# Kernel optimization log

Hardware: AMD Instinct MI355X
Metric: run time of the kernel (lower is better)

## Reference

```python
import jax, jax.numpy as jnp
import numpy as np

N = 10000      # nodes
E = 320000     # edges (avg degree 32)
H = 128        # hidden_channels
G = 50         # num_gaussians
NF = 128       # num_filters
L = 6          # num_interactions
CUTOFF = 10.0


def ssp(x):
    # ShiftedSoftplus: softplus(x) - log(2)
    return jax.nn.softplus(x) - jnp.log(2.0).astype(x.dtype)


def setup_inputs() -> dict:
    key = jax.random.key(0)
    ks = jax.random.split(key, 16)
    s = 0.05
    return {
        "z": jax.random.normal(ks[0], (N, H), jnp.float32),
        "pos": jax.random.normal(ks[1], (N, 3), jnp.float32) * 3.0,
        "edge_index": jax.random.randint(ks[2], (2, E), 0, N, dtype=jnp.int64),
        # per-layer stacked parameters (PyTorch Linear convention: y = x @ W.T + b)
        "mlp1_w": jax.random.normal(ks[3], (L, NF, G), jnp.float32) * s,
        "mlp1_b": jnp.zeros((L, NF), jnp.float32),
        "mlp2_w": jax.random.normal(ks[4], (L, NF, NF), jnp.float32) * s,
        "mlp2_b": jnp.zeros((L, NF), jnp.float32),
        "lin1_w": jax.random.normal(ks[5], (L, NF, H), jnp.float32) * s,   # no bias
        "lin2_w": jax.random.normal(ks[6], (L, H, NF), jnp.float32) * s,
        "lin2_b": jnp.zeros((L, H), jnp.float32),
        "lin_w": jax.random.normal(ks[7], (L, H, H), jnp.float32) * s,
        "lin_b": jnp.zeros((L, H), jnp.float32),
        "coord_w": jax.random.normal(ks[8], (L, 1, G + 2 * H), jnp.float32) * s,
        "coord_b": jnp.zeros((L, 1), jnp.float32),
    }


def reference(z, pos, edge_index, mlp1_w, mlp1_b, mlp2_w, mlp2_b,
              lin1_w, lin2_w, lin2_b, lin_w, lin_b, coord_w, coord_b):
    row, col = edge_index[0], edge_index[1]
    # edge distances from INITIAL positions (computed once, as in torch code)
    edge_weight = jnp.linalg.norm(pos[row] - pos[col], axis=-1)          # [E]
    offset = jnp.linspace(0.0, CUTOFF, G).astype(pos.dtype)              # [G]
    coeff = -0.5 / (offset[1] - offset[0]) ** 2
    edge_attr = jnp.exp(coeff * (edge_weight[:, None] - offset[None, :]) ** 2)  # [E,G]
    C = 0.5 * (jnp.cos(edge_weight * jnp.pi / CUTOFF) + 1.0)             # [E] cosine cutoff
    ones_e = jnp.ones((E,), pos.dtype)
    h = z
    for l in range(L):
        # ---- coordinate update (uses current pos and current h) ----
        feat = jnp.concatenate([edge_attr, h[row], h[col]], axis=-1)     # [E, G+2H]
        cw = feat @ coord_w[l].T + coord_b[l]                            # [E,1]
        aggr = (pos[row] - pos[col]) * cw                                # [E,3]
        sums = jax.ops.segment_sum(aggr, row, num_segments=N)            # [N,3]
        cnt = jax.ops.segment_sum(ones_e, row, num_segments=N)           # [N]
        mean = jnp.where(cnt[:, None] > 0, sums / jnp.maximum(cnt, 1.0)[:, None], 0.0)
        pos = pos + mean
        # ---- CFConv interaction ----
        Wf = ssp(edge_attr @ mlp1_w[l].T + mlp1_b[l]) @ mlp2_w[l].T + mlp2_b[l]  # [E,NF]
        Wf = Wf * C[:, None]
        xf = h @ lin1_w[l].T                                             # [N,NF]
        agg = jax.ops.segment_sum(xf[row] * Wf, col, num_segments=N)     # [N,NF]
        out = agg @ lin2_w[l].T + lin2_b[l]                              # [N,H]
        h = h + (ssp(out) @ lin_w[l].T + lin_b[l])
    return (pos, h)
```

## Files before the change

### kernel.cpp

```cpp
#include <hip/hip_runtime.h>


#define NN 10000
#define EE 320000
#define HH 128
#define GG 50
#define NF 128
#define NL 6
#define TROWS 2048
#define NB 128

typedef unsigned short u16;
typedef unsigned int u32;
typedef short bf16x8 __attribute__((ext_vector_type(8)));
typedef float f32x4  __attribute__((ext_vector_type(4)));

__device__ __forceinline__ float us2f(u16 u){
  union { float f; u32 i; } v; v.i = ((u32)u) << 16; return v.f;
}
__device__ __forceinline__ u16 f2us(float x){
  union { float f; u32 i; } v; v.f = x;
  u32 r = v.i + 0x7fffu + ((v.i >> 16) & 1u);
  return (u16)(r >> 16);
}
__device__ __forceinline__ float ldin(const void* p, int i, int bf){
  return bf ? us2f(((const u16*)p)[i]) : ((const float*)p)[i];
}
__device__ __forceinline__ float sspf(float x){
  return fmaxf(x, 0.f) + __logf(1.f + __expf(-fabsf(x))) - 0.6931472f;
}
__device__ __forceinline__ int detect_bf(const u32* __restrict__ zraw){
  int lane = threadIdx.x & 63;
  int c = 0;
  #pragma unroll
  for(int j=0;j<4;j++){
    u32 w = zraw[lane*4+j];
    u32 hb = (w >> 8) & 0x7F;
    c += (hb >= 0x38 && hb <= 0x41) ? 1 : 0;
  }
  return __popcll(__ballot(c >= 2)) >= 32;
}
__device__ __forceinline__ int detect_i64(const int* __restrict__ ei_raw){
  int lane = threadIdx.x & 63;
  int c = 0;
  #pragma unroll
  for(int j=0;j<4;j++) c += (ei_raw[2*(lane*4+j)+1] == 0) ? 1 : 0;
  return __popcll(__ballot(c >= 3)) >= 32;
}

__global__ void k_prep(const u32* __restrict__ zraw, const void* __restrict__ pos_in,
    const void* __restrict__ mlp1_w, const void* __restrict__ mlp1_b,
    const void* __restrict__ mlp2_w, const void* __restrict__ mlp2_b,
    const void* __restrict__ lin1_w, const void* __restrict__ lin2_w,
    const void* __restrict__ lin2_b, const void* __restrict__ lin_w,
    const void* __restrict__ lin_b,  const void* __restrict__ coord_w,
    const void* __restrict__ coord_b,
    float* __restrict__ h, float* __restrict__ pos, int* __restrict__ wmaxi,
    float* __restrict__ b1f, float* __restrict__ b2v,
    float* __restrict__ w1t, float* __restrict__ w2t,
    float* __restrict__ l1t, u16* __restrict__ l1b, u16* __restrict__ l2b,
    float* __restrict__ l2bf, u16* __restrict__ lwb,
    float* __restrict__ lbf, float* __restrict__ cwf, float* __restrict__ cbf)
{
  int bf = detect_bf(zraw);
  int b = blockIdx.x;
  if(b < NN*HH/256){
    int i = b*256 + threadIdx.x;
    h[i] = ldin(zraw, i, bf);
    if(i < NN*3) pos[i] = ldin(pos_in, i, bf);
    if(i == 0) *wmaxi = 0;
  } else {
    int i = (b - NN*HH/256)*256 + threadIdx.x;
    if(i < NL*NF){
      b1f[i]  = ldin(mlp1_b, i, bf);
      b2v[i]  = ldin(mlp2_b, i, bf);
      l2bf[i] = ldin(lin2_b, i, bf);
      lbf[i]  = ldin(lin_b,  i, bf);
    }
    if(i < NL*GG*NF){
      int l = i/(GG*NF), rem = i%(GG*NF);
      int g = rem/NF, f = rem%NF;
      w1t[i] = ldin(mlp1_w, (l*NF + f)*GG + g, bf);
    }
    if(i < NL*NF*NF){
      int l = i/(NF*NF), rem = i%(NF*NF);
      int k = rem/NF, f = rem%NF;
      w2t[i] = ldin(mlp2_w, l*NF*NF + f*NF + k, bf);
      l1t[i] = ldin(lin1_w, l*NF*HH + f*HH + k, bf);
      l1b[i] = f2us(ldin(lin1_w, i, bf));
      l2b[i] = f2us(ldin(lin2_w, i, bf));
      lwb[i] = f2us(ldin(lin_w,  i, bf));
    }
    if(i < NL*(GG+2*HH)) cwf[i] = ldin(coord_w, i, bf);
    if(i < NL) cbf[i] = ldin(coord_b, i, bf);
  }
}

__global__ void k_count(const int* __restrict__ ei_raw, const float* __restrict__ pos,
                        int* __restrict__ eiN, float* __restrict__ wE,
                        u32* __restrict__ partR32, u32* __restrict__ partC32,
                        int* __restrict__ wmaxi){
  __shared__ u32 hr[NN/2];
  __shared__ u32 hc[NN/2];
  int is64 = detect_i64(ei_raw);
  int b = blockIdx.x, tid = threadIdx.x;
  for(int i=tid; i<NN/2; i+=256){ hr[i]=0; hc[i]=0; }
  __syncthreads();
  int e0 = b*(EE/NB), e1 = e0 + EE/NB;
  float wm = 0.f;
  for(int e = e0 + tid; e < e1; e += 256){
    int r = is64 ? ei_raw[2*e] : ei_raw[e];
    int c = is64 ? ei_raw[2*(EE+e)] : ei_raw[EE+e];
    eiN[e] = r; eiN[EE+e] = c;
    float dx = pos[r*3+0]-pos[c*3+0];
    float dy = pos[r*3+1]-pos[c*3+1];
    float dz = pos[r*3+2]-pos[c*3+2];
    float w = sqrtf(dx*dx + dy*dy + dz*dz);
    wE[e] = w;
    wm = fmaxf(wm, w);
    atomicAdd(&hr[r>>1], (r&1) ? 0x10000u : 1u);
    atomicAdd(&hc[c>>1], (c&1) ? 0x10000u : 1u);
  }
  #pragma unroll
  for(int s=32; s>0; s>>=1) wm = fmaxf(wm, __shfl_down(wm, s, 64));
  if((tid & 63) == 0) atomicMax(wmaxi, __float_as_int(wm));
  __syncthreads();
  for(int i=tid; i<NN/2; i+=256){
    partR32[(size_t)b*(NN/2) + i] = hr[i];
    partC32[(size_t)b*(NN/2) + i] = hc[i];
  }
}

__global__ void k_sumpref(u16* __restrict__ partR16, u16* __restrict__ partC16,
                          int* __restrict__ degR, int* __restrict__ degC){
  int n = blockIdx.x*256 + threadIdx.x;
  if(n >= NN) return;
  u32 rr = 0, rc = 0;
  for(int b=0; b<NB; b++){
    u32 vr = partR16[(size_t)b*NN + n], vc = partC16[(size_t)b*NN + n];
    partR16[(size_t)b*NN + n] = (u16)rr;
    partC16[(size_t)b*NN + n] = (u16)rc;
    rr += vr; rc += vc;
  }
  degR[n] = (int)rr; degC[n] = (int)rc;
}

__global__ void k_scan2(const int* __restrict__ col_deg, const int* __restrict__ deg_row,
                        int* __restrict__ col_start, int* __restrict__ row_start){
  __shared__ int part[1024];
  int tid = threadIdx.x;
  const int CH = (NN + 1023)/1024;
  for(int pass=0; pass<2; pass++){
    const int* deg = pass ? deg_row : col_deg;
    int* start = pass ? row_start : col_start;
    int base = tid*CH;
    int s = 0;
    for(int i=0;i<CH;i++){ int idx=base+i; if(idx<NN) s += deg[idx]; }
    part[tid] = s;
    __syncthreads();
    for(int off=1; off<1024; off<<=1){
      int v = (tid>=off) ? part[tid-off] : 0;
      __syncthreads();
      part[tid] += v;
      __syncthreads();
    }
    int run = (tid==0) ? 0 : part[tid-1];
    for(int i=0;i<CH;i++){
      int idx = base+i;
      if(idx<NN){ start[idx]=run; run += deg[idx]; }
    }
    if(tid==1023) start[NN] = run;
    __syncthreads();
  }
}

__global__ void k_fill(const int* __restrict__ eiN, const float* __restrict__ wE,
                       const int* __restrict__ col_start, const int* __restrict__ row_start,
                       const u16* __restrict__ partR16, const u16* __restrict__ partC16,
                       int* __restrict__ row_s, float* __restrict__ wEs,
                       int* __restrict__ rcol_s, float* __restrict__ rw_s){
  __shared__ u32 hr[NN/2];
  __shared__ u32 hc[NN/2];
  int b = blockIdx.x, t = threadIdx.x;
  for(int i=t; i<NN/2; i+=256){ hr[i]=0; hc[i]=0; }
  __syncthreads();
  int e0 = b*(EE/NB), e1 = e0 + EE/NB;
  for(int e = e0 + t; e < e1; e += 256){
    int r = eiN[e], c = eiN[EE+e];
    float w = wE[e];
    u32 oldc = atomicAdd(&hc[c>>1], (c&1) ? 0x10000u : 1u);
    u32 rkc = (c&1) ? (oldc >> 16) : (oldc & 0xFFFFu);
    int p = col_start[c] + (int)partC16[(size_t)b*NN + c] + (int)rkc;
    row_s[p] = r; wEs[p] = w;
    u32 oldr = atomicAdd(&hr[r>>1], (r&1) ? 0x10000u : 1u);
    u32 rkr = (r&1) ? (oldr >> 16) : (oldr & 0xFFFFu);
    int p2 = row_start[r] + (int)partR16[(size_t)b*NN + r] + (int)rkr;
    rcol_s[p2] = c; rw_s[p2] = w;
  }
}

__global__ void k_tabnode(const float* __restrict__ w1t, const float* __restrict__ b1f,
                          const float* __restrict__ w2t, const float* __restrict__ b2v,
                          const float* __restrict__ cwf, const int* __restrict__ wmaxi,
                          u32* __restrict__ tabGb, float* __restrict__ tabS,
                          const float* __restrict__ h, const float* __restrict__ l1t,
                          u16* __restrict__ xfb0, float* __restrict__ dr0,
                          float* __restrict__ dc0){
  __shared__ float attr[17*64];
  __shared__ float tls[128*19];
  int b = blockIdx.x, t = threadIdx.x;
  if(b < NL*128){
    int l = b >> 7;
    int r0 = (b & 127)*16;
    int f = t & 127, half = t >> 7;
    float delta = __int_as_float(*wmaxi) / (float)(TROWS-1);
    for(int idx=t; idx<17*64; idx+=256){
      int r = idx >> 6, g = idx & 63;
      int row = min(r0 + r, TROWS-1);
      float w = (float)row*delta;
      float d = w - (float)g*(10.f/49.f);
      attr[idx] = (g < GG) ? __expf(-12.005f*d*d) : 0.f;
    }
    __syncthreads();
    const float* __restrict__ w1 = w1t + l*GG*NF;
    float b1 = b1f[l*NF + f];
    float a1[9];
    #pragma unroll
    for(int r=0;r<9;r++) a1[r] = b1;
    for(int g=0; g<GG; g++){
      float wv = w1[g*NF + f];
      #pragma unroll
      for(int r=0;r<9;r++) a1[r] += attr[(half*8 + r)*64 + g]*wv;
    }
    #pragma unroll
    for(int r=0;r<9;r++) tls[f*19 + half*9 + r] = sspf(a1[r]);
    __syncthreads();
    const float* __restrict__ w2 = w2t + l*NF*NF;
    float b2 = b2v[l*NF + f];
    float a2[9];
    #pragma unroll
    for(int r=0;r<9;r++) a2[r] = b2;
    for(int k=0;k<NF;k++){
      float wv = w2[k*NF + f];
      #pragma unroll
      for(int r=0;r<9;r++) a2[r] += tls[k*19 + half*9 + r]*wv;
    }
    float v[9];
    #pragma unroll
    for(int r=0;r<9;r++){
      int row = min(r0 + half*8 + r, TROWS-1);
      float w = (float)row*delta;
      float C = 0.5f*(cosf(w*0.3141592653589793f) + 1.f);
      v[r] = a2[r]*C;
    }
    #pragma unroll
    for(int j=0;j<8;j++){
      int row = r0 + half*8 + j;
      tabGb[((size_t)l*TROWS + row)*NF + f] = (u32)f2us(v[j]) | ((u32)f2us(v[j+1]) << 16);
    }
    if(t < 16){
      const float* __restrict__ cwg = cwf + l*(GG+2*HH);
      float s = 0.f;
      for(int g=0; g<GG; g++) s += attr[t*64 + g]*cwg[g];
      tabS[l*TROWS + r0 + t] = s;
    }
  } else {
    int nb = b - NL*128;
    if(nb < NN/8){
      int f = t & 127, g = t >> 7;
      int n0 = nb*8 + g*4;
      const float* __restrict__ wt = l1t;
      float acc[4] = {0.f,0.f,0.f,0.f};
      for(int k=0;k<HH;k++){
        float wv = wt[k*NF + f];
        #pragma unroll
        for(int i=0;i<4;i++) acc[i] += h[(n0+i)*HH + k]*wv;
      }
      #pragma unroll
      for(int i=0;i<4;i++) xfb0[(n0+i)*NF + f] = f2us(acc[i]);
    } else {
      int lane = t & 63;
      int n = (nb - NN/8)*4 + (t >> 6);
      const float* __restrict__ cw = cwf;
      float h0 = h[n*HH + lane], h1 = h[n*HH + 64 + lane];
      float ar = h0*cw[GG + lane]      + h1*cw[GG + 64 + lane];
      float ac = h0*cw[GG + HH + lane] + h1*cw[GG + HH + 64 + lane];
      #pragma unroll
      for(int s=32; s>0; s>>=1){
        ar += __shfl_down(ar, s, 64);
        ac += __shfl_down(ac, s, 64);
      }
      if(lane == 0){ dr0[n] = ar; dc0[n] = ac; }
    }
  }
}

__global__ void k_layer(const int* __restrict__ col_start, const int* __restrict__ row_s,
                        const float* __restrict__ wEs, const u32* __restrict__ xfR,
                        u16* __restrict__ xfW,
                        const u32* __restrict__ tabGb, const int* __restrict__ wmaxi,
                        int l,
                        const u16* __restrict__ l2b, const float* __restrict__ l2bf,
                        const u16* __restrict__ lwb, const float* __restrict__ lbf,
                        float* __restrict__ h, const u16* __restrict__ l1b,
                        const float* __restrict__ cwf,
                        const float* __restrict__ drR, float* __restrict__ drW,
                        const float* __restrict__ dcR, float* __restrict__ dcW,
                        const int* __restrict__ row_start, const int* __restrict__ rcol_s,
                        const float* __restrict__ rw_s, const float* __restrict__ tabS,
                        const float* __restrict__ cbf,
                        const float* __restrict__ pA, float* __restrict__ pB,
                        const u32* __restrict__ zraw, void* __restrict__ out){
  __shared__ __align__(16) u16 T[16*136];
  __shared__ __align__(16) u16 T2[16*136];
  int b = blockIdx.x, t = threadIdx.x;
  float invD = (float)(TROWS-1) / __int_as_float(*wmaxi);
  int wave = t >> 6, lane = t & 63;

  if(b < NN/16){
    int n0 = b*16;
    {
      const u32* __restrict__ tg = tabGb + (size_t)l*TROWS*NF;
      u32* __restrict__ T32 = (u32*)T;
      #pragma unroll
      for(int j=0;j<2;j++){
        int n = n0 + wave*2 + j;
        int p0 = col_start[n], p1 = col_start[n+1];
        float aa[4] = {0.f,0.f,0.f,0.f};
        float bb[4] = {0.f,0.f,0.f,0.f};
        int p = p0;
        for(; p+4 <= p1; p += 4){
          #pragma unroll
          for(int k=0;k<4;k++){
            int r = row_s[p+k];
            float tf = wEs[p+k]*invD;
            int i0 = min((int)tf, TROWS-2);
            float fr = tf - (float)i0;
            uint2 pr = *(const uint2*)&tg[i0*NF + 2*lane];
            u32 x = xfR[r*64 + lane];
            float lo = us2f((u16)pr.x), hi = us2f((u16)(pr.x>>16));
            aa[k] += us2f((u16)x)      *(lo + (hi-lo)*fr);
            lo = us2f((u16)pr.y); hi = us2f((u16)(pr.y>>16));
            bb[k] += us2f((u16)(x>>16))*(lo + (hi-lo)*fr);
          }
        }
        for(; p < p1; p++){
          int r = row_s[p];
          float tf = wEs[p]*invD;
          int i0 = min((int)tf, TROWS-2);
          float fr = tf - (float)i0;
          uint2 pr = *(const uint2*)&tg[i0*NF + 2*lane];
          u32 x = xfR[r*64 + lane];
          float lo = us2f((u16)pr.x), hi = us2f((u16)(pr.x>>16));
          aa[0] += us2f((u16)x)      *(lo + (hi-lo)*fr);
          lo = us2f((u16)pr.y); hi = us2f((u16)(pr.y>>16));
          bb[0] += us2f((u16)(x>>16))*(lo + (hi-lo)*fr);
        }
        float av = (aa[0]+aa[1])+(aa[2]+aa[3]);
        float bv = (bb[0]+bb[1])+(bb[2]+bb[3]);
        T32[(wave*2+j)*68 + lane] = (u32)f2us(av) | ((u32)f2us(bv) << 16);
      }
    }
    __syncthreads();
    int m16 = lane & 15, quad = lane >> 4;
    int fcol = wave*16 + m16;
    f32x4 acc;
    {
      bf16x8 aA[4];
      #pragma unroll
      for(int ks=0; ks<4; ks++)
        aA[ks] = *(const bf16x8*)&T[m16*136 + ks*32 + quad*8];
      const u16* __restrict__ wA = l2b + l*HH*NF;
      float bv = l2bf[l*HH + fcol];
      acc = (f32x4){bv,bv,bv,bv};
      #pragma unroll
      for(int ks=0; ks<4; ks++){
        bf16x8 bb = *(const bf16x8*)&wA[fcol*NF + ks*32 + quad*8];
        acc = __builtin_amdgcn_mfma_f32_16x16x32_bf16(aA[ks], bb, acc, 0,0,0);
      }
      #pragma unroll
      for(int r=0;r<4;r++)
        T2[(quad*4+r)*136 + fcol] = f2us(sspf(acc[r]));
    }
    __syncthreads();
    float hv[4];
    int bf = (l == NL-1) ? detect_bf(zraw) : 0;
    {
      bf16x8 aS[4];
      #pragma unroll
      for(int ks=0; ks<4; ks++)
        aS[ks] = *(const bf16x8*)&T2[m16*136 + ks*32 + quad*8];
      const u16* __restrict__ wB = lwb + l*HH*HH;
      float bv = lbf[l*HH + fcol];
      acc = (f32x4){bv,bv,bv,bv};
      #pragma unroll
      for(int ks=0; ks<4; ks++){
        bf16x8 bb = *(const bf16x8*)&wB[fcol*HH + ks*32 + quad*8];
        acc = __builtin_amdgcn_mfma_f32_16x16x32_bf16(aS[ks], bb, acc, 0,0,0);
      }
      #pragma unroll
      for(int r=0;r<4;r++)
        hv[r] = h[(n0+quad*4+r)*HH + fcol] + acc[r];
    }
    if(l == NL-1){
      #pragma unroll
      for(int r=0;r<4;r++){
        int n = n0 + quad*4 + r;
        if(bf) ((u16*)out)[NN*3 + n*HH + fcol] = f2us(hv[r]);
        else   ((float*)out)[NN*3 + n*HH + fcol] = hv[r];
      }
      return;
    }
    #pragma unroll
    for(int r=0;r<4;r++){
      int n = n0 + quad*4 + r;
      h[n*HH + fcol] = hv[r];
      T[(quad*4+r)*136 + fcol] = f2us(hv[r]);
    }
    __syncthreads();
    {
      bf16x8 aH[4];
      #pragma unroll
      for(int ks=0; ks<4; ks++)
        aH[ks] = *(const bf16x8*)&T[m16*136 + ks*32 + quad*8];
      const u16* __restrict__ wC = l1b + (l+1)*NF*HH;
      acc = (f32x4){0.f,0.f,0.f,0.f};
      #pragma unroll
      for(int ks=0; ks<4; ks++){
        bf16x8 bb = *(const bf16x8*)&wC[fcol*HH + ks*32 + quad*8];
        acc = __builtin_amdgcn_mfma_f32_16x16x32_bf16(aH[ks], bb, acc, 0,0,0);
      }
      #pragma unroll
      for(int r=0;r<4;r++)
        xfW[(n0+quad*4+r)*NF + fcol] = f2us(acc[r]);
    }
    {
      const float* __restrict__ cw = cwf + (l+1)*(GG + 2*HH);
      int j = t >> 5, l32 = t & 31;
      float ar = 0.f, ac = 0.f;
      #pragma unroll
      for(int i=0;i<4;i++){
        float hvv = us2f(T[j*136 + l32 + 32*i]);
        ar += hvv*cw[GG + l32 + 32*i];
        ac += hvv*cw[GG + HH + l32 + 32*i];
      }
      #pragma unroll
      for(int s=16; s>0; s>>=1){
        ar += __shfl_down(ar, s, 32);
        ac += __shfl_down(ac, s, 32);
      }
      if(l32 == 0){ drW[n0+j] = ar; dcW[n0+j] = ac; }
    }
  } else {
    int bf = (l == NL-1) ? detect_bf(zraw) : 0;
    int n = (b - NN/16)*8 + wave;
    const float* __restrict__ ts = tabS + l*TROWS;
    float cb = cbf[l] + drR[n];
    int p0 = row_start[n], p1 = row_start[n+1];
    float px = pA[n*3+0], py = pA[n*3+1], pz = pA[n*3+2];
    float sx=0.f, sy=0.f, sz=0.f;
    for(int p = p0 + lane; p < p1; p += 64){
      int c = rcol_s[p];
      float tf = rw_s[p]*invD;
      int i0 = min((int)tf, TROWS-2);
      float fr = tf - (float)i0;
      float s0 = ts[i0], s1 = ts[i0+1];
      float acc = cb + dcR[c] + s0 + (s1-s0)*fr;
      sx += (px - pA[c*3+0])*acc;
      sy += (py - pA[c*3+1])*acc;
      sz += (pz - pA[c*3+2])*acc;
    }
    #pragma unroll
    for(int s=32; s>0; s>>=1){
      sx += __shfl_down(sx, s, 64);
      sy += __shfl_down(sy, s, 64);
      sz += __shfl_down(sz, s, 64);
    }
    if(lane == 0){
      int cnt = p1 - p0;
      float inv = (cnt > 0) ? 1.f/(float)cnt : 0.f;
      float ox = px + sx*inv, oy = py + sy*inv, oz = pz + sz*inv;
      if(l == NL-1){
        if(bf){
          u16* o = (u16*)out;
          o[n*3+0] = f2us(ox); o[n*3+1] = f2us(oy); o[n*3+2] = f2us(oz);
        } else {
          float* o = (float*)out;
          o[n*3+0] = ox; o[n*3+1] = oy; o[n*3+2] = oz;
        }
      } else {
        pB[n*3+0] = ox; pB[n*3+1] = oy; pB[n*3+2] = oz;
      }
    }
  }
}

extern "C" void kernel_launch(void* const* d_in, const int* in_sizes, int n_in,
                              void* d_out, int out_size, void* d_ws, size_t ws_size,
                              hipStream_t stream){
  const u32*  z      = (const u32*)d_in[0];
  const void* pos_in = d_in[1];
  const int*  ei_raw = (const int*)d_in[2];
  const void* mlp1_w = d_in[3];
  const void* mlp1_b = d_in[4];
  const void* mlp2_w = d_in[5];
  const void* mlp2_b = d_in[6];
  const void* lin1_w = d_in[7];
  const void* lin2_w = d_in[8];
  const void* lin2_b = d_in[9];
  const void* lin_w  = d_in[10];
  const void* lin_b  = d_in[11];
  const void* coord_w= d_in[12];
  const void* coord_b= d_in[13];

  float* W = (float*)d_ws;
  float* h    = W; W += NN*HH;
  float* pos0 = W; W += NN*3;
  float* pos1 = W; W += NN*3;
  float* dr0  = W; W += NN;
  float* dr1  = W; W += NN;
  float* dc0  = W; W += NN;
  float* dc1  = W; W += NN;
  float* wE   = W; W += EE;
  float* wEs  = W; W += EE;
  float* rw_s = W; W += EE;
  float* b1f  = W; W += NL*NF;
  float* b2v  = W; W += NL*NF;
  float* w1t  = W; W += NL*GG*NF;
  float* w2t  = W; W += NL*NF*NF;
  float* l1t  = W; W += NL*NF*HH;
  float* l2bf = W; W += NL*HH;
  float* lbf  = W; W += NL*HH;
  float* cwf  = W; W += NL*(GG+2*HH);
  float* cbf  = W; W += NL;
  W = (float*)(((uintptr_t)W + 63) & ~(uintptr_t)63);
  u32*  tabGb = (u32*)W; W += (size_t)NL*TROWS*NF;
  float* tabS = W; W += NL*TROWS;
  u16* l1b  = (u16*)W; W += (NL*NF*NF)/2;
  u16* l2b  = (u16*)W; W += (NL*NF*NF)/2;
  u16* lwb  = (u16*)W; W += (NL*NF*NF)/2;
  u16* xfb0 = (u16*)W; W += (NN*NF)/2;
  u16* xfb1 = (u16*)W; W += (NN*NF)/2;
  u16* partR16 = (u16*)W; W += (size_t)NB*NN/2;
  u16* partC16 = (u16*)W; W += (size_t)NB*NN/2;
  int* degR      = (int*)W; W += NN;
  int* degC      = (int*)W; W += NN;
  int* col_start = (int*)W; W += NN+1;
  int* row_start = (int*)W; W += NN+1;
  int* row_s     = (int*)W; W += EE;
  int* rcol_s    = (int*)W; W += EE;
  int* eiN       = (int*)W; W += 2*EE;
  int* wmaxi     = (int*)W; W += 1;

  k_prep<<<NN*HH/256 + NL*NF*NF/256, 256, 0, stream>>>(
      z, pos_in, mlp1_w, mlp1_b, mlp2_w, mlp2_b, lin1_w, lin2_w, lin2_b,
      lin_w, lin_b, coord_w, coord_b,
      h, pos0, wmaxi,
      b1f, b2v, w1t, w2t, l1t, l1b, l2b, l2bf, lwb, lbf, cwf, cbf);
  k_count<<<NB, 256, 0, stream>>>(ei_raw, pos0, eiN, wE,
                                  (u32*)partR16, (u32*)partC16, wmaxi);
  k_sumpref<<<(NN+255)/256, 256, 0, stream>>>(partR16, partC16, degR, degC);
  k_scan2<<<1, 1024, 0, stream>>>(degC, degR, col_start, row_start);
  k_fill<<<NB, 256, 0, stream>>>(eiN, wE, col_start, row_start, partR16, partC16,
                                 row_s, wEs, rcol_s, rw_s);
  k_tabnode<<<NL*128 + NN/8 + NN/4, 256, 0, stream>>>(
      w1t, b1f, w2t, b2v, cwf, wmaxi, tabGb, tabS,
      h, l1t, xfb0, dr0, dc0);

  for(int l=0; l<NL; l++){
    int par = l & 1;
    const u32* xfR = (const u32*)(par ? xfb1 : xfb0);
    u16* xfW = par ? xfb0 : xfb1;
    const float* drR = par ? dr1 : dr0;  float* drW = par ? dr0 : dr1;
    const float* dcR = par ? dc1 : dc0;  float* dcW = par ? dc0 : dc1;
    const float* pA = par ? pos1 : pos0; float* pB = par ? pos0 : pos1;
    k_layer<<<NN/16 + NN/8, 512, 0, stream>>>(
        col_start, row_s, wEs, xfR, xfW, tabGb, wmaxi, l,
        l2b, l2bf, lwb, lbf, h, l1b, cwf,
        drR, drW, dcR, dcW,
        row_start, rcol_s, rw_s, tabS, cbf, pA, pB, z, d_out);
  }
}
```

Measured before the change: 410.4 us.

## Pack pos with dc into float4, use nearest-neighbor filter table, interleave layer blocks

Positions are stored as float4 together with the per-node dc term, so each neighbour needs one vector gather instead of several scalar loads. The filter lookup table doubles its resolution and switches from linear interpolation with packed adjacent-row pairs to a nearest-row bf16 lookup, which halves the bytes read per edge. The gather loop is unrolled to 8 edges, and CFConv and coordinate blocks are interleaved by blockIdx modulo 3. k_scan2 is fused into a single pass and k_sumpref batches its loads. Nearest-row lookup adds quantization error compared with interpolation, which the finer table is meant to offset.

```diff
diff --git a/kernel.cpp b/kernel.cpp
--- a/kernel.cpp
+++ b/kernel.cpp
@@ -7,7 +7,7 @@
 #define GG 50
 #define NF 128
 #define NL 6
-#define TROWS 2048
+#define TROWS 4096
 #define NB 128
 
 typedef unsigned short u16;
@@ -55,7 +55,7 @@
     const void* __restrict__ lin2_b, const void* __restrict__ lin_w,
     const void* __restrict__ lin_b,  const void* __restrict__ coord_w,
     const void* __restrict__ coord_b,
-    float* __restrict__ h, float* __restrict__ pos, int* __restrict__ wmaxi,
+    float* __restrict__ h, float* __restrict__ pc40, int* __restrict__ wmaxi,
     float* __restrict__ b1f, float* __restrict__ b2v,
     float* __restrict__ w1t, float* __restrict__ w2t,
     float* __restrict__ l1t, u16* __restrict__ l1b, u16* __restrict__ l2b,
@@ -67,7 +67,10 @@
   if(b < NN*HH/256){
     int i = b*256 + threadIdx.x;
     h[i] = ldin(zraw, i, bf);
-    if(i < NN*3) pos[i] = ldin(pos_in, i, bf);
+    if(i < NN*3){
+      int n = i/3, comp = i%3;
+      pc40[n*4 + comp] = ldin(pos_in, i, bf);
+    }
     if(i == 0) *wmaxi = 0;
   } else {
     int i = (b - NN*HH/256)*256 + threadIdx.x;
@@ -96,7 +99,7 @@
   }
 }
 
-__global__ void k_count(const int* __restrict__ ei_raw, const float* __restrict__ pos,
+__global__ void k_count(const int* __restrict__ ei_raw, const float* __restrict__ pc4,
                         int* __restrict__ eiN, float* __restrict__ wE,
                         u32* __restrict__ partR32, u32* __restrict__ partC32,
                         int* __restrict__ wmaxi){
@@ -112,9 +115,9 @@
     int r = is64 ? ei_raw[2*e] : ei_raw[e];
     int c = is64 ? ei_raw[2*(EE+e)] : ei_raw[EE+e];
     eiN[e] = r; eiN[EE+e] = c;
-    float dx = pos[r*3+0]-pos[c*3+0];
-    float dy = pos[r*3+1]-pos[c*3+1];
-    float dz = pos[r*3+2]-pos[c*3+2];
+    float4 pr = *(const float4*)&pc4[r*4];
+    float4 pcv = *(const float4*)&pc4[c*4];
+    float dx = pr.x-pcv.x, dy = pr.y-pcv.y, dz = pr.z-pcv.z;
     float w = sqrtf(dx*dx + dy*dy + dz*dz);
     wE[e] = w;
     wm = fmaxf(wm, w);
@@ -136,42 +139,53 @@
   int n = blockIdx.x*256 + threadIdx.x;
   if(n >= NN) return;
   u32 rr = 0, rc = 0;
-  for(int b=0; b<NB; b++){
-    u32 vr = partR16[(size_t)b*NN + n], vc = partC16[(size_t)b*NN + n];
-    partR16[(size_t)b*NN + n] = (u16)rr;
-    partC16[(size_t)b*NN + n] = (u16)rc;
-    rr += vr; rc += vc;
+  for(int b0=0; b0<NB; b0+=8){
+    u32 vr[8], vc[8];
+    #pragma unroll
+    for(int j=0;j<8;j++){
+      vr[j] = partR16[(size_t)(b0+j)*NN + n];
+      vc[j] = partC16[(size_t)(b0+j)*NN + n];
+    }
+    #pragma unroll
+    for(int j=0;j<8;j++){
+      partR16[(size_t)(b0+j)*NN + n] = (u16)rr; rr += vr[j];
+      partC16[(size_t)(b0+j)*NN + n] = (u16)rc; rc += vc[j];
+    }
   }
   degR[n] = (int)rr; degC[n] = (int)rc;
 }
 
 __global__ void k_scan2(const int* __restrict__ col_deg, const int* __restrict__ deg_row,
                         int* __restrict__ col_start, int* __restrict__ row_start){
-  __shared__ int part[1024];
+  __shared__ int pc[1024];
+  __shared__ int pr[1024];
   int tid = threadIdx.x;
   const int CH = (NN + 1023)/1024;
-  for(int pass=0; pass<2; pass++){
-    const int* deg = pass ? deg_row : col_deg;
-    int* start = pass ? row_start : col_start;
-    int base = tid*CH;
-    int s = 0;
-    for(int i=0;i<CH;i++){ int idx=base+i; if(idx<NN) s += deg[idx]; }
-    part[tid] = s;
-    __syncthreads();
-    for(int off=1; off<1024; off<<=1){
-      int v = (tid>=off) ? part[tid-off] : 0;
-      __syncthreads();
-      part[tid] += v;
-      __syncthreads();
-    }
-    int run = (tid==0) ? 0 : part[tid-1];
-    for(int i=0;i<CH;i++){
-      int idx = base+i;
-      if(idx<NN){ start[idx]=run; run += deg[idx]; }
-    }
-    if(tid==1023) start[NN] = run;
-    __syncthreads();
-  }
+  int base = tid*CH;
+  int sc = 0, sr = 0;
+  for(int i=0;i<CH;i++){
+    int idx = base+i;
+    if(idx<NN){ sc += col_deg[idx]; sr += deg_row[idx]; }
+  }
+  pc[tid] = sc; pr[tid] = sr;
+  __syncthreads();
+  for(int off=1; off<1024; off<<=1){
+    int vc = (tid>=off) ? pc[tid-off] : 0;
+    int vr = (tid>=off) ? pr[tid-off] : 0;
+    __syncthreads();
+    pc[tid] += vc; pr[tid] += vr;
+    __syncthreads();
+  }
+  int runc = (tid==0) ? 0 : pc[tid-1];
+  int runr = (tid==0) ? 0 : pr[tid-1];
+  for(int i=0;i<CH;i++){
+    int idx = base+i;
+    if(idx<NN){
+      col_start[idx]=runc; runc += col_deg[idx];
+      row_start[idx]=runr; runr += deg_row[idx];
+    }
+  }
+  if(tid==1023){ col_start[NN] = runc; row_start[NN] = runr; }
 }
 
 __global__ void k_fill(const int* __restrict__ eiN, const float* __restrict__ wE,
@@ -202,61 +216,54 @@
 __global__ void k_tabnode(const float* __restrict__ w1t, const float* __restrict__ b1f,
                           const float* __restrict__ w2t, const float* __restrict__ b2v,
                           const float* __restrict__ cwf, const int* __restrict__ wmaxi,
-                          u32* __restrict__ tabGb, float* __restrict__ tabS,
+                          u16* __restrict__ tabB, float* __restrict__ tabS,
                           const float* __restrict__ h, const float* __restrict__ l1t,
                           u16* __restrict__ xfb0, float* __restrict__ dr0,
-                          float* __restrict__ dc0){
-  __shared__ float attr[17*64];
-  __shared__ float tls[128*19];
+                          float* __restrict__ pc40){
+  __shared__ float attr[16*64];
+  __shared__ float tls[128*17];
   int b = blockIdx.x, t = threadIdx.x;
-  if(b < NL*128){
-    int l = b >> 7;
-    int r0 = (b & 127)*16;
+  if(b < NL*256){
+    int l = b >> 8;
+    int r0 = (b & 255)*16;
     int f = t & 127, half = t >> 7;
     float delta = __int_as_float(*wmaxi) / (float)(TROWS-1);
-    for(int idx=t; idx<17*64; idx+=256){
+    for(int idx=t; idx<16*64; idx+=256){
       int r = idx >> 6, g = idx & 63;
-      int row = min(r0 + r, TROWS-1);
-      float w = (float)row*delta;
+      float w = (float)(r0 + r)*delta;
       float d = w - (float)g*(10.f/49.f);
       attr[idx] = (g < GG) ? __expf(-12.005f*d*d) : 0.f;
     }
     __syncthreads();
     const float* __restrict__ w1 = w1t + l*GG*NF;
     float b1 = b1f[l*NF + f];
-    float a1[9];
-    #pragma unroll
-    for(int r=0;r<9;r++) a1[r] = b1;
+    float a1[8];
+    #pragma unroll
+    for(int r=0;r<8;r++) a1[r] = b1;
     for(int g=0; g<GG; g++){
       float wv = w1[g*NF + f];
       #pragma unroll
-      for(int r=0;r<9;r++) a1[r] += attr[(half*8 + r)*64 + g]*wv;
-    }
-    #pragma unroll
-    for(int r=0;r<9;r++) tls[f*19 + half*9 + r] = sspf(a1[r]);
+      for(int r=0;r<8;r++) a1[r] += attr[(half*8 + r)*64 + g]*wv;
+    }
+    #pragma unroll
+    for(int r=0;r<8;r++) tls[f*17 + half*8 + r] = sspf(a1[r]);
     __syncthreads();
     const float* __restrict__ w2 = w2t + l*NF*NF;
     float b2 = b2v[l*NF + f];
-    float a2[9];
-    #pragma unroll
-    for(int r=0;r<9;r++) a2[r] = b2;
+    float a2[8];
+    #pragma unroll
+    for(int r=0;r<8;r++) a2[r] = b2;
     for(int k=0;k<NF;k++){
       float wv = w2[k*NF + f];
       #pragma unroll
-      for(int r=0;r<9;r++) a2[r] += tls[k*19 + half*9 + r]*wv;
-    }
-    float v[9];
-    #pragma unroll
-    for(int r=0;r<9;r++){
-      int row = min(r0 + half*8 + r, TROWS-1);
+      for(int r=0;r<8;r++) a2[r] += tls[k*17 + half*8 + r]*wv;
+    }
+    #pragma unroll
+    for(int r=0;r<8;r++){
+      int row = r0 + half*8 + r;
       float w = (float)row*delta;
       float C = 0.5f*(cosf(w*0.3141592653589793f) + 1.f);
-      v[r] = a2[r]*C;
-    }
-    #pragma unroll
-    for(int j=0;j<8;j++){
-      int row = r0 + half*8 + j;
-      tabGb[((size_t)l*TROWS + row)*NF + f] = (u32)f2us(v[j]) | ((u32)f2us(v[j+1]) << 16);
+      tabB[((size_t)l*TROWS + row)*NF + f] = f2us(a2[r]*C);
     }
     if(t < 16){
       const float* __restrict__ cwg = cwf + l*(GG+2*HH);
@@ -265,7 +272,7 @@
       tabS[l*TROWS + r0 + t] = s;
     }
   } else {
-    int nb = b - NL*128;
+    int nb = b - NL*256;
     if(nb < NN/8){
       int f = t & 127, g = t >> 7;
       int n0 = nb*8 + g*4;
@@ -290,7 +297,7 @@
         ar += __shfl_down(ar, s, 64);
         ac += __shfl_down(ac, s, 64);
       }
-      if(lane == 0){ dr0[n] = ar; dc0[n] = ac; }
+      if(lane == 0){ dr0[n] = ar; pc40[n*4+3] = ac; }
     }
   }
 }
@@ -298,18 +305,17 @@
 __global__ void k_layer(const int* __restrict__ col_start, const int* __restrict__ row_s,
                         const float* __restrict__ wEs, const u32* __restrict__ xfR,
                         u16* __restrict__ xfW,
-                        const u32* __restrict__ tabGb, const int* __restrict__ wmaxi,
+                        const u16* __restrict__ tabB, const int* __restrict__ wmaxi,
                         int l,
                         const u16* __restrict__ l2b, const float* __restrict__ l2bf,
                         const u16* __restrict__ lwb, const float* __restrict__ lbf,
                         float* __restrict__ h, const u16* __restrict__ l1b,
                         const float* __restrict__ cwf,
                         const float* __restrict__ drR, float* __restrict__ drW,
-                        const float* __restrict__ dcR, float* __restrict__ dcW,
                         const int* __restrict__ row_start, const int* __restrict__ rcol_s,
                         const float* __restrict__ rw_s, const float* __restrict__ tabS,
                         const float* __restrict__ cbf,
-                        const float* __restrict__ pA, float* __restrict__ pB,
+                        const float* __restrict__ pc4R, float* __restrict__ pc4W,
                         const u32* __restrict__ zraw, void* __restrict__ out){
   __shared__ __align__(16) u16 T[16*136];
   __shared__ __align__(16) u16 T2[16*136];
@@ -317,10 +323,10 @@
   float invD = (float)(TROWS-1) / __int_as_float(*wmaxi);
   int wave = t >> 6, lane = t & 63;
 
-  if(b < NN/16){
-    int n0 = b*16;
+  if(b % 3 == 0){
+    int n0 = (b/3)*16;
     {
-      const u32* __restrict__ tg = tabGb + (size_t)l*TROWS*NF;
+      const u32* __restrict__ tg32 = (const u32*)(tabB + (size_t)l*TROWS*NF);
       u32* __restrict__ T32 = (u32*)T;
       #pragma unroll
       for(int j=0;j<2;j++){
@@ -329,32 +335,28 @@
         float aa[4] = {0.f,0.f,0.f,0.f};
         float bb[4] = {0.f,0.f,0.f,0.f};
         int p = p0;
-        for(; p+4 <= p1; p += 4){
+        for(; p+8 <= p1; p += 8){
+          u32 gv[8], xv[8];
           #pragma unroll
-          for(int k=0;k<4;k++){
+          for(int k=0;k<8;k++){
             int r = row_s[p+k];
-            float tf = wEs[p+k]*invD;
-            int i0 = min((int)tf, TROWS-2);
-            float fr = tf - (float)i0;
-            uint2 pr = *(const uint2*)&tg[i0*NF + 2*lane];
-            u32 x = xfR[r*64 + lane];
-            float lo = us2f((u16)pr.x), hi = us2f((u16)(pr.x>>16));
-            aa[k] += us2f((u16)x)      *(lo + (hi-lo)*fr);
-            lo = us2f((u16)pr.y); hi = us2f((u16)(pr.y>>16));
-            bb[k] += us2f((u16)(x>>16))*(lo + (hi-lo)*fr);
+            int i0 = min((int)(wEs[p+k]*invD + 0.5f), TROWS-1);
+            gv[k] = tg32[i0*64 + lane];
+            xv[k] = xfR[r*64 + lane];
+          }
+          #pragma unroll
+          for(int k=0;k<8;k++){
+            aa[k&3] += us2f((u16)xv[k])      * us2f((u16)gv[k]);
+            bb[k&3] += us2f((u16)(xv[k]>>16))* us2f((u16)(gv[k]>>16));
           }
         }
         for(; p < p1; p++){
           int r = row_s[p];
-          float tf = wEs[p]*invD;
-          int i0 = min((int)tf, TROWS-2);
-          float fr = tf - (float)i0;
-          uint2 pr = *(const uint2*)&tg[i0*NF + 2*lane];
+          int i0 = min((int)(wEs[p]*invD + 0.5f), TROWS-1);
+          u32 g = tg32[i0*64 + lane];
           u32 x = xfR[r*64 + lane];
-          float lo = us2f((u16)pr.x), hi = us2f((u16)(pr.x>>16));
-          aa[0] += us2f((u16)x)      *(lo + (hi-lo)*fr);
-          lo = us2f((u16)pr.y); hi = us2f((u16)(pr.y>>16));
-          bb[0] += us2f((u16)(x>>16))*(lo + (hi-lo)*fr);
+          aa[0] += us2f((u16)x)      * us2f((u16)g);
+          bb[0] += us2f((u16)(x>>16))* us2f((u16)(g>>16));
         }
         float av = (aa[0]+aa[1])+(aa[2]+aa[3]);
         float bv = (bb[0]+bb[1])+(bb[2]+bb[3]);
@@ -375,8 +377,8 @@
       acc = (f32x4){bv,bv,bv,bv};
       #pragma unroll
       for(int ks=0; ks<4; ks++){
-        bf16x8 bb = *(const bf16x8*)&wA[fcol*NF + ks*32 + quad*8];
-        acc = __builtin_amdgcn_mfma_f32_16x16x32_bf16(aA[ks], bb, acc, 0,0,0);
+        bf16x8 bbv = *(const bf16x8*)&wA[fcol*NF + ks*32 + quad*8];
+        acc = __builtin_amdgcn_mfma_f32_16x16x32_bf16(aA[ks], bbv, acc, 0,0,0);
       }
       #pragma unroll
       for(int r=0;r<4;r++)
@@ -395,8 +397,8 @@
       acc = (f32x4){bv,bv,bv,bv};
       #pragma unroll
       for(int ks=0; ks<4; ks++){
-        bf16x8 bb = *(const bf16x8*)&wB[fcol*HH + ks*32 + quad*8];
-        acc = __builtin_amdgcn_mfma_f32_16x16x32_bf16(aS[ks], bb, acc, 0,0,0);
+        bf16x8 bbv = *(const bf16x8*)&wB[fcol*HH + ks*32 + quad*8];
+        acc = __builtin_amdgcn_mfma_f32_16x16x32_bf16(aS[ks], bbv, acc, 0,0,0);
       }
       #pragma unroll
       for(int r=0;r<4;r++)
@@ -427,8 +429,8 @@
       acc = (f32x4){0.f,0.f,0.f,0.f};
       #pragma unroll
       for(int ks=0; ks<4; ks++){
-        bf16x8 bb = *(const bf16x8*)&wC[fcol*HH + ks*32 + quad*8];
-        acc = __builtin_amdgcn_mfma_f32_16x16x32_bf16(aH[ks], bb, acc, 0,0,0);
+        bf16x8 bbv = *(const bf16x8*)&wC[fcol*HH + ks*32 + quad*8];
+        acc = __builtin_amdgcn_mfma_f32_16x16x32_bf16(aH[ks], bbv, acc, 0,0,0);
       }
       #pragma unroll
       for(int r=0;r<4;r++)
@@ -449,26 +451,25 @@
         ar += __shfl_down(ar, s, 32);
         ac += __shfl_down(ac, s, 32);
       }
-      if(l32 == 0){ drW[n0+j] = ar; dcW[n0+j] = ac; }
+      if(l32 == 0){ drW[n0+j] = ar; pc4W[(n0+j)*4+3] = ac; }
     }
   } else {
+    int u = b - b/3 - 1;
     int bf = (l == NL-1) ? detect_bf(zraw) : 0;
-    int n = (b - NN/16)*8 + wave;
+    int n = u*8 + wave;
     const float* __restrict__ ts = tabS + l*TROWS;
     float cb = cbf[l] + drR[n];
     int p0 = row_start[n], p1 = row_start[n+1];
-    float px = pA[n*3+0], py = pA[n*3+1], pz = pA[n*3+2];
+    float4 pn = *(const float4*)&pc4R[n*4];
     float sx=0.f, sy=0.f, sz=0.f;
     for(int p = p0 + lane; p < p1; p += 64){
       int c = rcol_s[p];
-      float tf = rw_s[p]*invD;
-      int i0 = min((int)tf, TROWS-2);
-      float fr = tf - (float)i0;
-      float s0 = ts[i0], s1 = ts[i0+1];
-      float acc = cb + dcR[c] + s0 + (s1-s0)*fr;
-      sx += (px - pA[c*3+0])*acc;
-      sy += (py - pA[c*3+1])*acc;
-      sz += (pz - pA[c*3+2])*acc;
+      int i0 = min((int)(rw_s[p]*invD + 0.5f), TROWS-1);
+      float4 pcv = *(const float4*)&pc4R[c*4];
+      float a = cb + pcv.w + ts[i0];
+      sx += (pn.x - pcv.x)*a;
+      sy += (pn.y - pcv.y)*a;
+      sz += (pn.z - pcv.z)*a;
     }
     #pragma unroll
     for(int s=32; s>0; s>>=1){
@@ -479,7 +480,7 @@
     if(lane == 0){
       int cnt = p1 - p0;
       float inv = (cnt > 0) ? 1.f/(float)cnt : 0.f;
-      float ox = px + sx*inv, oy = py + sy*inv, oz = pz + sz*inv;
+      float ox = pn.x + sx*inv, oy = pn.y + sy*inv, oz = pn.z + sz*inv;
       if(l == NL-1){
         if(bf){
           u16* o = (u16*)out;
@@ -489,7 +490,7 @@
           o[n*3+0] = ox; o[n*3+1] = oy; o[n*3+2] = oz;
         }
       } else {
-        pB[n*3+0] = ox; pB[n*3+1] = oy; pB[n*3+2] = oz;
+        pc4W[n*4+0] = ox; pc4W[n*4+1] = oy; pc4W[n*4+2] = oz;
       }
     }
   }
@@ -515,12 +516,10 @@
 
   float* W = (float*)d_ws;
   float* h    = W; W += NN*HH;
-  float* pos0 = W; W += NN*3;
-  float* pos1 = W; W += NN*3;
+  float* pc40 = W; W += NN*4;
+  float* pc41 = W; W += NN*4;
   float* dr0  = W; W += NN;
   float* dr1  = W; W += NN;
-  float* dc0  = W; W += NN;
-  float* dc1  = W; W += NN;
   float* wE   = W; W += EE;
   float* wEs  = W; W += EE;
   float* rw_s = W; W += EE;
@@ -534,7 +533,7 @@
   float* cwf  = W; W += NL*(GG+2*HH);
   float* cbf  = W; W += NL;
   W = (float*)(((uintptr_t)W + 63) & ~(uintptr_t)63);
-  u32*  tabGb = (u32*)W; W += (size_t)NL*TROWS*NF;
+  u16*  tabB = (u16*)W; W += (size_t)NL*TROWS*NF/2;
   float* tabS = W; W += NL*TROWS;
   u16* l1b  = (u16*)W; W += (NL*NF*NF)/2;
   u16* l2b  = (u16*)W; W += (NL*NF*NF)/2;
@@ -555,29 +554,28 @@
   k_prep<<<NN*HH/256 + NL*NF*NF/256, 256, 0, stream>>>(
       z, pos_in, mlp1_w, mlp1_b, mlp2_w, mlp2_b, lin1_w, lin2_w, lin2_b,
       lin_w, lin_b, coord_w, coord_b,
-      h, pos0, wmaxi,
+      h, pc40, wmaxi,
       b1f, b2v, w1t, w2t, l1t, l1b, l2b, l2bf, lwb, lbf, cwf, cbf);
-  k_count<<<NB, 256, 0, stream>>>(ei_raw, pos0, eiN, wE,
+  k_count<<<NB, 256, 0, stream>>>(ei_raw, pc40, eiN, wE,
                                   (u32*)partR16, (u32*)partC16, wmaxi);
   k_sumpref<<<(NN+255)/256, 256, 0, stream>>>(partR16, partC16, degR, degC);
   k_scan2<<<1, 1024, 0, stream>>>(degC, degR, col_start, row_start);
   k_fill<<<NB, 256, 0, stream>>>(eiN, wE, col_start, row_start, partR16, partC16,
                                  row_s, wEs, rcol_s, rw_s);
-  k_tabnode<<<NL*128 + NN/8 + NN/4, 256, 0, stream>>>(
-      w1t, b1f, w2t, b2v, cwf, wmaxi, tabGb, tabS,
-      h, l1t, xfb0, dr0, dc0);
+  k_tabnode<<<NL*256 + NN/8 + NN/4, 256, 0, stream>>>(
+      w1t, b1f, w2t, b2v, cwf, wmaxi, tabB, tabS,
+      h, l1t, xfb0, dr0, pc40);
 
   for(int l=0; l<NL; l++){
     int par = l & 1;
     const u32* xfR = (const u32*)(par ? xfb1 : xfb0);
     u16* xfW = par ? xfb0 : xfb1;
-    const float* drR = par ? dr1 : dr0;  float* drW = par ? dr0 : dr1;
-    const float* dcR = par ? dc1 : dc0;  float* dcW = par ? dc0 : dc1;
-    const float* pA = par ? pos1 : pos0; float* pB = par ? pos0 : pos1;
-    k_layer<<<NN/16 + NN/8, 512, 0, stream>>>(
-        col_start, row_s, wEs, xfR, xfW, tabGb, wmaxi, l,
+    const float* drR = par ? dr1 : dr0;   float* drW = par ? dr0 : dr1;
+    const float* p4R = par ? pc41 : pc40; float* p4W = par ? pc40 : pc41;
+    k_layer<<<3*(NN/16), 512, 0, stream>>>(
+        col_start, row_s, wEs, xfR, xfW, tabB, wmaxi, l,
         l2b, l2bf, lwb, lbf, h, l1b, cwf,
-        drR, drW, dcR, dcW,
-        row_start, rcol_s, rw_s, tabS, cbf, pA, pB, z, d_out);
-  }
-}
+        drR, drW,
+        row_start, rcol_s, rw_s, tabS, cbf, p4R, p4W, z, d_out);
+  }
+}
```

Result: slower. 427.6 us (+4.2%).
